# Optimization experiments

Hardware: AMD Instinct MI355X
Metric: run time of the kernel (lower is better)

Reference implementation:

```python
import jax, jax.numpy as jnp
from jax import lax
import numpy as np

C, CK, CV, K = 256, 32, 32, 3  # channels, key_channels, value_channels, kernel_size
B, H, W = 8, 128, 128


def setup_inputs() -> dict:
    key = jax.random.key(0)
    ks = jax.random.split(key, 12)
    s = 0.05
    return {
        "x": jax.random.normal(ks[0], (B, C, H, W), jnp.float32),
        # key branch: 1x1 conv C->CK (+ReLU), depthwise 3x3 CK->CK, 1x1 conv CK->K*K
        "k1_w": jax.random.normal(ks[1], (CK, C), jnp.float32) * s,
        "k1_b": jax.random.normal(ks[2], (CK,), jnp.float32) * s,
        "dw_w": jax.random.normal(ks[3], (CK, 1, K, K), jnp.float32) * s,
        "dw_b": jax.random.normal(ks[4], (CK,), jnp.float32) * s,
        "k3_w": jax.random.normal(ks[5], (K * K, CK), jnp.float32) * s,
        "k3_b": jax.random.normal(ks[6], (K * K,), jnp.float32) * s,
        # value branch: 1x1 conv C->CV (no act)
        "v_w": jax.random.normal(ks[7], (CV, C), jnp.float32) * s,
        "v_b": jax.random.normal(ks[8], (CV,), jnp.float32) * s,
        # out conv: 1x1 CV->C (no act)
        "o_w": jax.random.normal(ks[9], (C, CV), jnp.float32) * s,
        "o_b": jax.random.normal(ks[10], (C,), jnp.float32) * s,
    }


def _conv1x1(t, w, b):
    # t: [B,Cin,H,W], w: [Cout,Cin] -> [B,Cout,H,W]
    return jnp.einsum("bchw,oc->bohw", t, w) + b[None, :, None, None]


def reference(x, k1_w, k1_b, dw_w, dw_b, k3_w, k3_b, v_w, v_b, o_w, o_b):
    b, _, h, w = x.shape
    pad = (K - 1) // 2
    # ---- key branch ----
    k = jax.nn.relu(_conv1x1(x, k1_w, k1_b))
    k = lax.conv_general_dilated(
        k, dw_w, window_strides=(1, 1), padding=[(pad, pad), (pad, pad)],
        dimension_numbers=("NCHW", "OIHW", "NCHW"), feature_group_count=CK,
    ) + dw_b[None, :, None, None]
    k = _conv1x1(k, k3_w, k3_b)                      # [B, K*K, H, W]
    weights = jax.nn.softmax(k, axis=1)[:, None]     # [B, 1, K*K, H, W]
    # ---- value branch: 1x1 conv then unfold (3x3 neighborhoods, pad 1) ----
    v = _conv1x1(x, v_w, v_b)                        # [B, CV, H, W]
    vp = jnp.pad(v, ((0, 0), (0, 0), (pad, pad), (pad, pad)))
    # torch Unfold ordering: per-channel, kernel offsets row-major
    patches = jnp.stack(
        [vp[:, :, i : i + h, j : j + w] for i in range(K) for j in range(K)],
        axis=2,
    )                                                # [B, CV, K*K, H, W]
    y = jnp.sum(weights * patches, axis=2)           # [B, CV, H, W]
    y = _conv1x1(y, o_w, o_b)                        # [B, C, H, W]
    return x + y
```

## Files before the change

### kernel.cpp

```cpp
#include <hip/hip_runtime.h>
#include <cmath>

namespace {
constexpr int Cc = 256, CKc = 32, CVc = 32, KKc = 9;
constexpr int Bc = 8, Hc = 128, Wc = 128, HWc = Hc * Wc;

typedef __attribute__((ext_vector_type(8))) short   s16x8;
typedef __attribute__((ext_vector_type(8))) __bf16  bf16x8;
typedef __attribute__((ext_vector_type(4))) float   f32x4;

__device__ inline short f2bf(float f) {
    union { float f; unsigned u; } v; v.f = f;
    unsigned u = v.u + 0x7fffu + ((v.u >> 16) & 1u);
    return (short)(u >> 16);
}
}

__global__ __launch_bounds__(256) void ns_k1v(
    const float* __restrict__ x,
    const float* __restrict__ k1_w, const float* __restrict__ k1_b,
    const float* __restrict__ v_w,  const float* __restrict__ v_b,
    float* __restrict__ k1, float* __restrict__ v)
{
    constexpr int LP = 72;
    __shared__ short w_bf[64][LP];
    __shared__ short x_bf[128][LP];

    const int tid = threadIdx.x;
    const int l   = tid & 63;
    const int li  = l & 15;
    const int lk  = l >> 4;
    const int wv  = __builtin_amdgcn_readfirstlane(tid >> 6);

    const int flat0 = blockIdx.x * 128;
    const int b  = flat0 / HWc;
    const int pp = flat0 - b * HWc;
    const float* xb = x + (size_t)b * Cc * HWc + pp;

    const int spx  = tid & 127;
    const int schh = tid >> 7;
    const int so   = tid & 63;
    const int swc0 = (tid >> 6) * 16;
    const float* wsrc = (so < 32) ? (k1_w + (size_t)so * Cc)
                                  : (v_w + (size_t)(so - 32) * Cc);

    f32x4 acc[8];
    const f32x4 zero = {0.f, 0.f, 0.f, 0.f};
#pragma unroll
    for (int i = 0; i < 8; ++i) acc[i] = zero;

    for (int c0 = 0; c0 < Cc; c0 += 64) {
        __syncthreads();
        {
            alignas(16) short tmp[16];
#pragma unroll
            for (int f = 0; f < 4; ++f) {
                const float4 fv = *(const float4*)(wsrc + c0 + swc0 + f * 4);
                tmp[f*4+0] = f2bf(fv.x); tmp[f*4+1] = f2bf(fv.y);
                tmp[f*4+2] = f2bf(fv.z); tmp[f*4+3] = f2bf(fv.w);
            }
            *(s16x8*)&w_bf[so][swc0]     = *(const s16x8*)&tmp[0];
            *(s16x8*)&w_bf[so][swc0 + 8] = *(const s16x8*)&tmp[8];
        }
#pragma unroll
        for (int u = 0; u < 8; ++u) {
            const int ch = (schh * 8 + u) * 4;
            const float e0 = xb[(size_t)(c0 + ch + 0) * HWc + spx];
            const float e1 = xb[(size_t)(c0 + ch + 1) * HWc + spx];
            const float e2 = xb[(size_t)(c0 + ch + 2) * HWc + spx];
            const float e3 = xb[(size_t)(c0 + ch + 3) * HWc + spx];
            const unsigned p01 = (unsigned)(unsigned short)f2bf(e0)
                               | ((unsigned)(unsigned short)f2bf(e1) << 16);
            const unsigned p23 = (unsigned)(unsigned short)f2bf(e2)
                               | ((unsigned)(unsigned short)f2bf(e3) << 16);
            *(uint2*)&x_bf[spx][ch] = make_uint2(p01, p23);
        }
        __syncthreads();

#pragma unroll
        for (int ks = 0; ks < 2; ++ks) {
            const s16x8 ar = *(const s16x8*)&w_bf[wv * 16 + li][ks * 32 + lk * 8];
            const bf16x8 af = __builtin_bit_cast(bf16x8, ar);
#pragma unroll
            for (int pt = 0; pt < 8; ++pt) {
                const s16x8 br = *(const s16x8*)&x_bf[pt * 16 + li][ks * 32 + lk * 8];
                acc[pt] = __builtin_amdgcn_mfma_f32_16x16x32_bf16(
                    af, __builtin_bit_cast(bf16x8, br), acc[pt], 0, 0, 0);
            }
        }
    }

    const bool is_k = wv < 2;
    const int obase = wv * 16 + lk * 4;
    float bias[4];
#pragma unroll
    for (int r = 0; r < 4; ++r)
        bias[r] = is_k ? k1_b[obase + r] : v_b[obase + r - 32];
    float* dst0 = is_k ? (k1 + ((size_t)b * CKc + obase) * HWc + pp)
                       : (v  + ((size_t)b * CVc + (obase - 32)) * HWc + pp);
#pragma unroll
    for (int pt = 0; pt < 8; ++pt) {
        const int px = pt * 16 + li;
#pragma unroll
        for (int r = 0; r < 4; ++r) {
            float val = acc[pt][r] + bias[r];
            if (is_k) val = fmaxf(val, 0.f);
            dst0[(size_t)r * HWc + px] = val;
        }
    }
}

__global__ __launch_bounds__(128) void ns_fused(
    const float* __restrict__ x,
    const float* __restrict__ k1,
    const float* __restrict__ v,
    const float* __restrict__ dw_w, const float* __restrict__ dw_b,
    const float* __restrict__ k3_w, const float* __restrict__ k3_b,
    const float* __restrict__ o_w,  const float* __restrict__ o_b,
    float* __restrict__ out)
{
    constexpr int PX = 128;
    constexpr int WPAD = 40;
    __shared__ short w_lds[Cc][WPAD];
    __shared__ short y_lds[PX][WPAD];
    __shared__ float obs[Cc];
    __shared__ float dwt[KKc][CKc];
    __shared__ float k3s[KKc][CKc];
    __shared__ float dwbs[CKc];
    __shared__ float k3bs[KKc];

    const int tid = threadIdx.x;

#pragma unroll
    for (int r = 0; r < 2; ++r) {
        const int o = tid + r * 128;
        const float* src = o_w + o * CVc;
        alignas(16) short tmp[CVc];
#pragma unroll
        for (int c = 0; c < CVc; c += 4) {
            const float4 f = *(const float4*)(src + c);
            tmp[c+0] = f2bf(f.x); tmp[c+1] = f2bf(f.y);
            tmp[c+2] = f2bf(f.z); tmp[c+3] = f2bf(f.w);
        }
#pragma unroll
        for (int cq = 0; cq < 4; ++cq)
            *(float4*)&w_lds[o][cq * 8] = *(const float4*)&tmp[cq * 8];
        obs[o] = o_b[o];
    }
    for (int idx = tid; idx < CKc * KKc; idx += 128) {
        const int ck = idx / KKc, kk = idx - ck * KKc;
        dwt[kk][ck] = dw_w[idx];
        ((float*)k3s)[idx] = k3_w[idx];
    }
    if (tid < CKc) dwbs[tid] = dw_b[tid];
    if (tid < KKc) k3bs[tid] = k3_b[tid];
    __syncthreads();

    const int flat0 = blockIdx.x * PX;
    const int b  = flat0 / HWc;
    const int p0 = flat0 - b * HWc;
    const int p  = p0 + tid;
    const int h  = p / Wc;
    const int w  = p - h * Wc;

    const float* k1b = k1 + (size_t)b * CKc * HWc;
    float t[CKc];
#pragma unroll
    for (int ck = 0; ck < CKc; ++ck) t[ck] = dwbs[ck];
#pragma unroll
    for (int i = 0; i < 3; ++i) {
        const int hh = h + i - 1;
        if (hh < 0 || hh >= Hc) continue;
#pragma unroll
        for (int j = 0; j < 3; ++j) {
            const int ww = w + j - 1;
            if (ww < 0 || ww >= Wc) continue;
            const int off = hh * Wc + ww;
            const int ij = i * 3 + j;
#pragma unroll
            for (int ck = 0; ck < CKc; ++ck)
                t[ck] = fmaf(k1b[(size_t)ck * HWc + off], dwt[ij][ck], t[ck]);
        }
    }

    float logit[KKc];
#pragma unroll
    for (int kk = 0; kk < KKc; ++kk) {
        float a = k3bs[kk];
#pragma unroll
        for (int ck = 0; ck < CKc; ++ck)
            a = fmaf(k3s[kk][ck], t[ck], a);
        logit[kk] = a;
    }
    float m = logit[0];
#pragma unroll
    for (int kk = 1; kk < KKc; ++kk) m = fmaxf(m, logit[kk]);
    float s = 0.f;
#pragma unroll
    for (int kk = 0; kk < KKc; ++kk) { logit[kk] = expf(logit[kk] - m); s += logit[kk]; }
    const float inv = 1.f / s;
#pragma unroll
    for (int kk = 0; kk < KKc; ++kk) logit[kk] *= inv;

    float yv[CVc];
#pragma unroll
    for (int cv = 0; cv < CVc; ++cv) yv[cv] = 0.f;
    const float* vb = v + (size_t)b * CVc * HWc;
#pragma unroll
    for (int i = 0; i < 3; ++i) {
        const int hh = h + i - 1;
        if (hh < 0 || hh >= Hc) continue;
#pragma unroll
        for (int j = 0; j < 3; ++j) {
            const int ww = w + j - 1;
            if (ww < 0 || ww >= Wc) continue;
            const int off = hh * Wc + ww;
            const float wv = logit[i * 3 + j];
#pragma unroll
            for (int cv = 0; cv < CVc; ++cv)
                yv[cv] = fmaf(wv, vb[(size_t)cv * HWc + off], yv[cv]);
        }
    }

    {
        alignas(16) short ybf[CVc];
#pragma unroll
        for (int cv = 0; cv < CVc; ++cv) ybf[cv] = f2bf(yv[cv]);
#pragma unroll
        for (int cq = 0; cq < 4; ++cq)
            *(float4*)&y_lds[tid][cq * 8] = *(const float4*)&ybf[cq * 8];
    }
    __syncthreads();

    const int wvv = tid >> 6;
    const int l  = tid & 63;
    const int li = l & 15;
    const int lk = l >> 4;

    const float* xb0 = x + (size_t)b * Cc * HWc;
    float* ob0 = out + (size_t)b * Cc * HWc;

    for (int ot = wvv * 8; ot < wvv * 8 + 8; ++ot) {
        const s16x8 araw = *(const s16x8*)&w_lds[ot * 16 + li][lk * 8];
        const bf16x8 afrag = __builtin_bit_cast(bf16x8, araw);
        const int obase = ot * 16 + lk * 4;
        const f32x4 bias = *(const f32x4*)&obs[obase];
#pragma unroll
        for (int pt = 0; pt < 8; ++pt) {
            const s16x8 braw = *(const s16x8*)&y_lds[pt * 16 + li][lk * 8];
            const bf16x8 bfrag = __builtin_bit_cast(bf16x8, braw);
            f32x4 acc = {0.f, 0.f, 0.f, 0.f};
            acc = __builtin_amdgcn_mfma_f32_16x16x32_bf16(afrag, bfrag, acc, 0, 0, 0);
            const int px = p0 + pt * 16 + li;
            const float* xp = xb0 + (size_t)obase * HWc + px;
            float* op = ob0 + (size_t)obase * HWc + px;
#pragma unroll
            for (int r = 0; r < 4; ++r)
                op[(size_t)r * HWc] = xp[(size_t)r * HWc] + acc[r] + bias[r];
        }
    }
}

extern "C" void kernel_launch(void* const* d_in, const int* in_sizes, int n_in,
                              void* d_out, int out_size, void* d_ws, size_t ws_size,
                              hipStream_t stream)
{
    const float* x    = (const float*)d_in[0];
    const float* k1_w = (const float*)d_in[1];
    const float* k1_b = (const float*)d_in[2];
    const float* dw_w = (const float*)d_in[3];
    const float* dw_b = (const float*)d_in[4];
    const float* k3_w = (const float*)d_in[5];
    const float* k3_b = (const float*)d_in[6];
    const float* v_w  = (const float*)d_in[7];
    const float* v_b  = (const float*)d_in[8];
    const float* o_w  = (const float*)d_in[9];
    const float* o_b  = (const float*)d_in[10];
    float* out = (float*)d_out;

    float* k1 = (float*)d_ws;
    float* v  = k1 + (size_t)Bc * CKc * HWc;

    const int npx = Bc * HWc;

    ns_k1v <<<dim3(npx / 128), dim3(256), 0, stream>>>(x, k1_w, k1_b, v_w, v_b, k1, v);
    ns_fused<<<dim3(npx / 128), dim3(128), 0, stream>>>(x, k1, v, dw_w, dw_b, k3_w, k3_b,
                                                        o_w, o_b, out);
}
```

Measured before the change: 102.3 us.

## Store intermediates as pixel-major bf16 and prestage bf16 out-conv weights

The first kernel now writes the key and value intermediates as bf16 in a pixel-major layout (32 channels contiguous per pixel) rather than channel-planar fp32. It also converts o_w to bf16 once, inside block 0. The fused kernel loads each neighbor's channels with 16-byte vector loads and reads the out-conv weights straight from global memory instead of staging them in LDS. Its block grows to 256 pixels and threads. This halves the intermediate traffic and removes per-block weight conversion, but the intermediates lose precision to bf16, and the o_w conversion in block 0 is not ordered against the reads in the second kernel except by stream order.

New measurement: 102.6 us. Within noise of the previous version (+0.2%).

```diff
diff --git a/kernel.cpp b/kernel.cpp
--- a/kernel.cpp
+++ b/kernel.cpp
@@ -9,10 +9,10 @@
 typedef __attribute__((ext_vector_type(8))) __bf16  bf16x8;
 typedef __attribute__((ext_vector_type(4))) float   f32x4;
 
-__device__ inline short f2bf(float f) {
+__device__ inline unsigned short f2bf(float f) {
     union { float f; unsigned u; } v; v.f = f;
     unsigned u = v.u + 0x7fffu + ((v.u >> 16) & 1u);
-    return (short)(u >> 16);
+    return (unsigned short)(u >> 16);
 }
 }
 
@@ -20,7 +20,9 @@
     const float* __restrict__ x,
     const float* __restrict__ k1_w, const float* __restrict__ k1_b,
     const float* __restrict__ v_w,  const float* __restrict__ v_b,
-    float* __restrict__ k1, float* __restrict__ v)
+    const float* __restrict__ o_w,
+    unsigned short* __restrict__ k1pm, unsigned short* __restrict__ vpm,
+    unsigned short* __restrict__ owbf)
 {
     constexpr int LP = 72;
     __shared__ short w_bf[64][LP];
@@ -31,6 +33,15 @@
     const int li  = l & 15;
     const int lk  = l >> 4;
     const int wv  = __builtin_amdgcn_readfirstlane(tid >> 6);
+
+    if (blockIdx.x == 0) {
+        for (int i = tid * 4; i < Cc * CVc; i += 256 * 4) {
+            const float4 f = *(const float4*)(o_w + i);
+            const unsigned a = (unsigned)f2bf(f.x) | ((unsigned)f2bf(f.y) << 16);
+            const unsigned c = (unsigned)f2bf(f.z) | ((unsigned)f2bf(f.w) << 16);
+            *(uint2*)(owbf + i) = make_uint2(a, c);
+        }
+    }
 
     const int flat0 = blockIdx.x * 128;
     const int b  = flat0 / HWc;
@@ -69,10 +80,8 @@
             const float e1 = xb[(size_t)(c0 + ch + 1) * HWc + spx];
             const float e2 = xb[(size_t)(c0 + ch + 2) * HWc + spx];
             const float e3 = xb[(size_t)(c0 + ch + 3) * HWc + spx];
-            const unsigned p01 = (unsigned)(unsigned short)f2bf(e0)
-                               | ((unsigned)(unsigned short)f2bf(e1) << 16);
-            const unsigned p23 = (unsigned)(unsigned short)f2bf(e2)
-                               | ((unsigned)(unsigned short)f2bf(e3) << 16);
+            const unsigned p01 = (unsigned)f2bf(e0) | ((unsigned)f2bf(e1) << 16);
+            const unsigned p23 = (unsigned)f2bf(e2) | ((unsigned)f2bf(e3) << 16);
             *(uint2*)&x_bf[spx][ch] = make_uint2(p01, p23);
         }
         __syncthreads();
@@ -92,62 +101,47 @@
 
     const bool is_k = wv < 2;
     const int obase = wv * 16 + lk * 4;
+    const int chq = is_k ? obase : obase - 32;
     float bias[4];
 #pragma unroll
     for (int r = 0; r < 4; ++r)
         bias[r] = is_k ? k1_b[obase + r] : v_b[obase + r - 32];
-    float* dst0 = is_k ? (k1 + ((size_t)b * CKc + obase) * HWc + pp)
-                       : (v  + ((size_t)b * CVc + (obase - 32)) * HWc + pp);
+    unsigned short* dstb = is_k ? k1pm : vpm;
+
 #pragma unroll
     for (int pt = 0; pt < 8; ++pt) {
-        const int px = pt * 16 + li;
-#pragma unroll
-        for (int r = 0; r < 4; ++r) {
-            float val = acc[pt][r] + bias[r];
-            if (is_k) val = fmaxf(val, 0.f);
-            dst0[(size_t)r * HWc + px] = val;
-        }
-    }
-}
-
-__global__ __launch_bounds__(128) void ns_fused(
+        const size_t row = (size_t)b * HWc + pp + pt * 16 + li;
+        float v0 = acc[pt][0] + bias[0], v1 = acc[pt][1] + bias[1];
+        float v2 = acc[pt][2] + bias[2], v3 = acc[pt][3] + bias[3];
+        if (is_k) {
+            v0 = fmaxf(v0, 0.f); v1 = fmaxf(v1, 0.f);
+            v2 = fmaxf(v2, 0.f); v3 = fmaxf(v3, 0.f);
+        }
+        const unsigned p01 = (unsigned)f2bf(v0) | ((unsigned)f2bf(v1) << 16);
+        const unsigned p23 = (unsigned)f2bf(v2) | ((unsigned)f2bf(v3) << 16);
+        *(uint2*)(dstb + row * 32 + chq) = make_uint2(p01, p23);
+    }
+}
+
+__global__ __launch_bounds__(256) void ns_fused(
     const float* __restrict__ x,
-    const float* __restrict__ k1,
-    const float* __restrict__ v,
+    const unsigned short* __restrict__ k1pm,
+    const unsigned short* __restrict__ vpm,
     const float* __restrict__ dw_w, const float* __restrict__ dw_b,
     const float* __restrict__ k3_w, const float* __restrict__ k3_b,
-    const float* __restrict__ o_w,  const float* __restrict__ o_b,
+    const unsigned short* __restrict__ owbf, const float* __restrict__ o_b,
     float* __restrict__ out)
 {
-    constexpr int PX = 128;
+    constexpr int PX = 256;
     constexpr int WPAD = 40;
-    __shared__ short w_lds[Cc][WPAD];
     __shared__ short y_lds[PX][WPAD];
-    __shared__ float obs[Cc];
     __shared__ float dwt[KKc][CKc];
     __shared__ float k3s[KKc][CKc];
     __shared__ float dwbs[CKc];
     __shared__ float k3bs[KKc];
 
     const int tid = threadIdx.x;
-
-#pragma unroll
-    for (int r = 0; r < 2; ++r) {
-        const int o = tid + r * 128;
-        const float* src = o_w + o * CVc;
-        alignas(16) short tmp[CVc];
-#pragma unroll
-        for (int c = 0; c < CVc; c += 4) {
-            const float4 f = *(const float4*)(src + c);
-            tmp[c+0] = f2bf(f.x); tmp[c+1] = f2bf(f.y);
-            tmp[c+2] = f2bf(f.z); tmp[c+3] = f2bf(f.w);
-        }
-#pragma unroll
-        for (int cq = 0; cq < 4; ++cq)
-            *(float4*)&w_lds[o][cq * 8] = *(const float4*)&tmp[cq * 8];
-        obs[o] = o_b[o];
-    }
-    for (int idx = tid; idx < CKc * KKc; idx += 128) {
+    for (int idx = tid; idx < CKc * KKc; idx += 256) {
         const int ck = idx / KKc, kk = idx - ck * KKc;
         dwt[kk][ck] = dw_w[idx];
         ((float*)k3s)[idx] = k3_w[idx];
@@ -163,23 +157,28 @@
     const int h  = p / Wc;
     const int w  = p - h * Wc;
 
-    const float* k1b = k1 + (size_t)b * CKc * HWc;
+    const unsigned short* k1b = k1pm + (size_t)b * HWc * 32;
+    const unsigned short* vb  = vpm  + (size_t)b * HWc * 32;
+
     float t[CKc];
 #pragma unroll
     for (int ck = 0; ck < CKc; ++ck) t[ck] = dwbs[ck];
 #pragma unroll
     for (int i = 0; i < 3; ++i) {
         const int hh = h + i - 1;
-        if (hh < 0 || hh >= Hc) continue;
 #pragma unroll
         for (int j = 0; j < 3; ++j) {
             const int ww = w + j - 1;
-            if (ww < 0 || ww >= Wc) continue;
-            const int off = hh * Wc + ww;
+            if (hh < 0 || hh >= Hc || ww < 0 || ww >= Wc) continue;
+            const unsigned short* kr = k1b + (size_t)(hh * Wc + ww) * 32;
             const int ij = i * 3 + j;
 #pragma unroll
-            for (int ck = 0; ck < CKc; ++ck)
-                t[ck] = fmaf(k1b[(size_t)ck * HWc + off], dwt[ij][ck], t[ck]);
+            for (int qv = 0; qv < 4; ++qv) {
+                const bf16x8 kv = __builtin_bit_cast(bf16x8, *(const s16x8*)(kr + qv * 8));
+#pragma unroll
+                for (int e = 0; e < 8; ++e)
+                    t[qv * 8 + e] = fmaf((float)kv[e], dwt[ij][qv * 8 + e], t[qv * 8 + e]);
+            }
         }
     }
 
@@ -205,27 +204,29 @@
     float yv[CVc];
 #pragma unroll
     for (int cv = 0; cv < CVc; ++cv) yv[cv] = 0.f;
-    const float* vb = v + (size_t)b * CVc * HWc;
 #pragma unroll
     for (int i = 0; i < 3; ++i) {
         const int hh = h + i - 1;
-        if (hh < 0 || hh >= Hc) continue;
 #pragma unroll
         for (int j = 0; j < 3; ++j) {
             const int ww = w + j - 1;
-            if (ww < 0 || ww >= Wc) continue;
-            const int off = hh * Wc + ww;
+            if (hh < 0 || hh >= Hc || ww < 0 || ww >= Wc) continue;
+            const unsigned short* vr = vb + (size_t)(hh * Wc + ww) * 32;
             const float wv = logit[i * 3 + j];
 #pragma unroll
-            for (int cv = 0; cv < CVc; ++cv)
-                yv[cv] = fmaf(wv, vb[(size_t)cv * HWc + off], yv[cv]);
+            for (int qv = 0; qv < 4; ++qv) {
+                const bf16x8 vv = __builtin_bit_cast(bf16x8, *(const s16x8*)(vr + qv * 8));
+#pragma unroll
+                for (int e = 0; e < 8; ++e)
+                    yv[qv * 8 + e] = fmaf(wv, (float)vv[e], yv[qv * 8 + e]);
+            }
         }
     }
 
     {
         alignas(16) short ybf[CVc];
 #pragma unroll
-        for (int cv = 0; cv < CVc; ++cv) ybf[cv] = f2bf(yv[cv]);
+        for (int cv = 0; cv < CVc; ++cv) ybf[cv] = (short)f2bf(yv[cv]);
 #pragma unroll
         for (int cq = 0; cq < 4; ++cq)
             *(float4*)&y_lds[tid][cq * 8] = *(const float4*)&ybf[cq * 8];
@@ -240,17 +241,19 @@
     const float* xb0 = x + (size_t)b * Cc * HWc;
     float* ob0 = out + (size_t)b * Cc * HWc;
 
-    for (int ot = wvv * 8; ot < wvv * 8 + 8; ++ot) {
-        const s16x8 araw = *(const s16x8*)&w_lds[ot * 16 + li][lk * 8];
-        const bf16x8 afrag = __builtin_bit_cast(bf16x8, araw);
+#pragma unroll
+    for (int i = 0; i < 4; ++i) {
+        const int ot = wvv * 4 + i;
+        const s16x8 ar = *(const s16x8*)(owbf + (size_t)(ot * 16 + li) * 32 + lk * 8);
+        const bf16x8 af = __builtin_bit_cast(bf16x8, ar);
         const int obase = ot * 16 + lk * 4;
-        const f32x4 bias = *(const f32x4*)&obs[obase];
-#pragma unroll
-        for (int pt = 0; pt < 8; ++pt) {
-            const s16x8 braw = *(const s16x8*)&y_lds[pt * 16 + li][lk * 8];
-            const bf16x8 bfrag = __builtin_bit_cast(bf16x8, braw);
+        const f32x4 bias = *(const f32x4*)(o_b + obase);
+#pragma unroll
+        for (int pt = 0; pt < 16; ++pt) {
+            const s16x8 br = *(const s16x8*)&y_lds[pt * 16 + li][lk * 8];
             f32x4 acc = {0.f, 0.f, 0.f, 0.f};
-            acc = __builtin_amdgcn_mfma_f32_16x16x32_bf16(afrag, bfrag, acc, 0, 0, 0);
+            acc = __builtin_amdgcn_mfma_f32_16x16x32_bf16(
+                af, __builtin_bit_cast(bf16x8, br), acc, 0, 0, 0);
             const int px = p0 + pt * 16 + li;
             const float* xp = xb0 + (size_t)obase * HWc + px;
             float* op = ob0 + (size_t)obase * HWc + px;
@@ -278,12 +281,14 @@
     const float* o_b  = (const float*)d_in[10];
     float* out = (float*)d_out;
 
-    float* k1 = (float*)d_ws;
-    float* v  = k1 + (size_t)Bc * CKc * HWc;
+    unsigned short* k1pm = (unsigned short*)d_ws;
+    unsigned short* vpm  = k1pm + (size_t)Bc * HWc * 32;
+    unsigned short* owbf = vpm  + (size_t)Bc * HWc * 32;
 
     const int npx = Bc * HWc;
 
-    ns_k1v <<<dim3(npx / 128), dim3(256), 0, stream>>>(x, k1_w, k1_b, v_w, v_b, k1, v);
-    ns_fused<<<dim3(npx / 128), dim3(128), 0, stream>>>(x, k1, v, dw_w, dw_b, k3_w, k3_b,
-                                                        o_w, o_b, out);
-}
+    ns_k1v <<<dim3(npx / 128), dim3(256), 0, stream>>>(x, k1_w, k1_b, v_w, v_b, o_w,
+                                                       k1pm, vpm, owbf);
+    ns_fused<<<dim3(npx / 256), dim3(256), 0, stream>>>(x, k1pm, vpm, dw_w, dw_b,
+                                                        k3_w, k3_b, owbf, o_b, out);
+}
```
